# Optimization experiments

Hardware: AMD Instinct MI355X
Metric: run time of the kernel (lower is better)

## Reference

```python
import jax, jax.numpy as jnp
import numpy as np

B, N, D = 4, 4096, 256
H = 4
HD = D // H
FF = max(2 * D, 16)
EPS = 1e-5


def layer_norm(x, w, b):
    mu = jnp.mean(x, axis=-1, keepdims=True)
    var = jnp.mean(jnp.square(x - mu), axis=-1, keepdims=True)
    return (x - mu) * jax.lax.rsqrt(var + EPS) * w + b


def setup_inputs() -> dict:
    key = jax.random.key(0)
    ks = jax.random.split(key, 12)
    s = 1.0 / np.sqrt(D)
    sf = 1.0 / np.sqrt(FF)
    return {
        "tokens": jax.random.normal(ks[0], (B, N, D), jnp.float32),
        "importance": jax.random.normal(ks[1], (B, N), jnp.float32),
        "norm1_w": jnp.ones((D,), jnp.float32),
        "norm1_b": jnp.zeros((D,), jnp.float32),
        "Wq": jax.random.uniform(ks[2], (D, D), jnp.float32, -s, s),
        "bq": jnp.zeros((D,), jnp.float32),
        "Wk": jax.random.uniform(ks[3], (D, D), jnp.float32, -s, s),
        "bk": jnp.zeros((D,), jnp.float32),
        "Wv": jax.random.uniform(ks[4], (D, D), jnp.float32, -s, s),
        "bv": jnp.zeros((D,), jnp.float32),
        "Wo": jax.random.uniform(ks[5], (D, D), jnp.float32, -s, s),
        "bo": jnp.zeros((D,), jnp.float32),
        "norm2_w": jnp.ones((D,), jnp.float32),
        "norm2_b": jnp.zeros((D,), jnp.float32),
        "W1": jax.random.uniform(ks[6], (D, FF), jnp.float32, -s, s),
        "b1": jnp.zeros((FF,), jnp.float32),
        "W2": jax.random.uniform(ks[7], (FF, D), jnp.float32, -sf, sf),
        "b2": jnp.zeros((D,), jnp.float32),
    }


def reference(tokens, importance, norm1_w, norm1_b, Wq, bq, Wk, bk, Wv, bv,
              Wo, bo, norm2_w, norm2_b, W1, b1, W2, b2):
    # pre-norm MHA with additive importance bias
    x = layer_norm(tokens, norm1_w, norm1_b)
    q = (x @ Wq + bq).reshape(B, N, H, HD).transpose(0, 2, 1, 3)  # [B,H,N,HD]
    k = (x @ Wk + bk).reshape(B, N, H, HD).transpose(0, 2, 1, 3)
    v = (x @ Wv + bv).reshape(B, N, H, HD).transpose(0, 2, 1, 3)
    scores = jnp.einsum("bhnd,bhmd->bhnm", q, k) / np.sqrt(HD)
    scores = scores + importance[:, None, None, :]  # bias over key dim
    attn = jax.nn.softmax(scores, axis=-1)
    ctx = jnp.einsum("bhnm,bhmd->bhnd", attn, v)
    ctx = ctx.transpose(0, 2, 1, 3).reshape(B, N, D)
    x = tokens + (ctx @ Wo + bo)
    # GELU FFN (exact erf gelu, matching torch default)
    y = layer_norm(x, norm2_w, norm2_b)
    y = jax.nn.gelu(y @ W1 + b1, approximate=False) @ W2 + b2
    return x + y
```

## Files before the change

kernel.cpp:

```cpp
#include <hip/hip_runtime.h>

#define Bb 4
#define Nn 4096
#define Dd 256
#define Hh 4
#define HDd 64
#define FFf 512
#define MT 16384

typedef __attribute__((ext_vector_type(8))) short short8;
typedef __attribute__((ext_vector_type(4))) float f32x4;
typedef __attribute__((ext_vector_type(16))) float f32x16;
typedef unsigned short u16;
typedef unsigned int u32;
typedef __attribute__((ext_vector_type(4))) u32 u32x4;

typedef __attribute__((address_space(1))) const void glb_src;
typedef __attribute__((address_space(3))) void lds_dst;

__device__ __forceinline__ void gload_lds16(const void* g, void* l) {
    __builtin_amdgcn_global_load_lds((glb_src*)g, (lds_dst*)l, 16, 0, 0);
}

__device__ __forceinline__ u16 f2bf(float f) {
    union { float f; u32 i; } v; v.f = f;
    u32 r = v.i + 0x7FFFu + ((v.i >> 16) & 1u);
    return (u16)(r >> 16);
}

__device__ __forceinline__ short8 ld8(const u16* p) {
    return *(const short8*)p;
}

__device__ __forceinline__ void pl32swap(u32& a, u32& b) {
    asm("v_permlane32_swap_b32 %0, %1" : "+v"(a), "+v"(b));
}
__device__ __forceinline__ float xhalf_max(float x) {
    u32 a = __float_as_uint(x), b = a;
    pl32swap(a, b);
    return fmaxf(__uint_as_float(a), __uint_as_float(b));
}
__device__ __forceinline__ u32 cvtpk(float lo, float hi) {
    u32 r;
    asm("v_cvt_pk_bf16_f32 %0, %1, %2" : "=v"(r) : "v"(lo), "v"(hi));
    return r;
}
__device__ __forceinline__ float fexp2(float x) {
    float r;
    asm("v_exp_f32 %0, %1" : "=v"(r) : "v"(x));
    return r;
}
__device__ __forceinline__ float max3f(float a, float b, float c) {
    float r;
    asm("v_max3_f32 %0, %1, %2, %3" : "=v"(r) : "v"(a), "v"(b), "v"(c));
    return r;
}

#define QSCALE 0.18033610062f
#define LOG2E  1.44269504089f

__global__ __launch_bounds__(256) void prep_kernel(
        const float* __restrict__ Wq, const float* __restrict__ Wk,
        const float* __restrict__ Wv, const float* __restrict__ Wo,
        const float* __restrict__ W1, const float* __restrict__ W2,
        const float* __restrict__ imp,
        u16* __restrict__ WqkvT, u16* __restrict__ WoT,
        u16* __restrict__ W1T, u16* __restrict__ W2T,
        u32* __restrict__ impPk) {
    int e = blockIdx.x * 256 + threadIdx.x;
    if (e < 196608) {
        int c = e >> 8, k = e & 255;
        int mat = c >> 8;
        int cc = c & 255;
        const float* W = (mat == 0) ? Wq : ((mat == 1) ? Wk : Wv);
        WqkvT[(size_t)c * 256 + k] = f2bf(W[k * 256 + cc]);
    } else if (e < 262144) {
        int i = e - 196608; int n = i >> 8, k = i & 255;
        WoT[n * 256 + k] = f2bf(Wo[k * 256 + n]);
    } else if (e < 393216) {
        int i = e - 262144; int n = i >> 8, k = i & 255;
        W1T[n * 256 + k] = f2bf(W1[k * 512 + n]);
    } else if (e < 524288) {
        int i = e - 393216; int n = i >> 9, k = i & 511;
        W2T[n * 512 + k] = f2bf(W2[k * 256 + n]);
    } else {
        int i = e - 524288;
        float ivs = imp[i] * LOG2E;
        u16 ih = f2bf(ivs);
        float rem = ivs - __uint_as_float(((u32)ih) << 16);
        u16 il = f2bf(rem);
        impPk[i] = ((u32)il << 16) | ih;
    }
}

__global__ __launch_bounds__(256) void ln_kernel(const float* __restrict__ x,
        const float* __restrict__ w, const float* __restrict__ bia,
        u16* __restrict__ out) {
    int lane = threadIdx.x & 63;
    int row = blockIdx.x * 4 + (threadIdx.x >> 6);
    const float* xr = x + (size_t)row * Dd;
    float4 v = *(const float4*)(xr + lane * 4);
    float s = v.x + v.y + v.z + v.w;
    float s2 = v.x * v.x + v.y * v.y + v.z * v.z + v.w * v.w;
    #pragma unroll
    for (int off = 1; off < 64; off <<= 1) {
        s  += __shfl_xor(s, off);
        s2 += __shfl_xor(s2, off);
    }
    float mu = s * (1.0f / Dd);
    float var = s2 * (1.0f / Dd) - mu * mu;
    float rstd = rsqrtf(var + 1e-5f);
    float4 wv = *(const float4*)(w + lane * 4);
    float4 bv = *(const float4*)(bia + lane * 4);
    ushort4 ov;
    ov.x = f2bf((v.x - mu) * rstd * wv.x + bv.x);
    ov.y = f2bf((v.y - mu) * rstd * wv.y + bv.y);
    ov.z = f2bf((v.z - mu) * rstd * wv.z + bv.z);
    ov.w = f2bf((v.w - mu) * rstd * wv.w + bv.w);
    *(ushort4*)(out + (size_t)row * Dd + lane * 4) = ov;
}

template<int MODE, int KD>
__global__ __launch_bounds__(256) void gemm_bt(
        const u16* __restrict__ A, const u16* __restrict__ BT,
        const float* __restrict__ bias0, const float* __restrict__ bias1,
        const float* __restrict__ bias2,
        const float* __restrict__ resid, float* __restrict__ outf,
        u16* __restrict__ o0, u16* __restrict__ o1, u16* __restrict__ o2) {
    __shared__ u16 Asl[128 * 32];
    __shared__ u16 Bsl[128 * 32];
    int lane = threadIdx.x & 63;
    int wv = threadIdx.x >> 6;
    int wm = wv >> 1, wn = wv & 1;
    int m0 = blockIdx.y * 128, n0 = blockIdx.x * 128;
    f32x4 zz; zz[0] = 0.f; zz[1] = 0.f; zz[2] = 0.f; zz[3] = 0.f;
    f32x4 acc[4][4];
    #pragma unroll
    for (int i = 0; i < 4; ++i)
        #pragma unroll
        for (int j = 0; j < 4; ++j) acc[i][j] = zz;

    for (int kt = 0; kt < KD; kt += 32) {
        __syncthreads();
        #pragma unroll
        for (int i = 0; i < 2; ++i) {
            int chunk = threadIdx.x + i * 256;
            int row = chunk >> 2, c16 = chunk & 3;
            int lofs = row * 32 + ((c16 * 8) ^ ((row & 3) * 8));
            *(uint4*)(Asl + lofs) = *(const uint4*)(A + (size_t)(m0 + row) * KD + kt + c16 * 8);
            *(uint4*)(Bsl + lofs) = *(const uint4*)(BT + (size_t)(n0 + row) * KD + kt + c16 * 8);
        }
        __syncthreads();
        short8 af[4], bfr[4];
        #pragma unroll
        for (int t = 0; t < 4; ++t) {
            int arow = wm * 64 + t * 16 + (lane & 15);
            af[t]  = ld8(Asl + arow * 32 + (((lane >> 4) * 8) ^ ((arow & 3) * 8)));
            int brow = wn * 64 + t * 16 + (lane & 15);
            bfr[t] = ld8(Bsl + brow * 32 + (((lane >> 4) * 8) ^ ((brow & 3) * 8)));
        }
        #pragma unroll
        for (int mt = 0; mt < 4; ++mt)
            #pragma unroll
            for (int nt = 0; nt < 4; ++nt)
                acc[mt][nt] = __builtin_amdgcn_mfma_f32_16x16x32_bf16(af[mt], bfr[nt], acc[mt][nt], 0, 0, 0);
    }

    #pragma unroll
    for (int mt = 0; mt < 4; ++mt) {
        #pragma unroll
        for (int nt = 0; nt < 4; ++nt) {
            #pragma unroll
            for (int r = 0; r < 4; ++r) {
                int row = m0 + wm * 64 + mt * 16 + (lane >> 4) * 4 + r;
                int col = n0 + wn * 64 + nt * 16 + (lane & 15);
                float v = acc[mt][nt][r];
                if (MODE == 0) {
                    int mat = col >> 8;
                    int cc = col & 255;
                    int hh = cc >> 6, dd = cc & 63;
                    int bbi = row >> 12, nni = row & 4095;
                    int bh = bbi * Hh + hh;
                    if (mat == 0)      o0[((size_t)bh * Nn + nni) * HDd + dd] = f2bf((v + bias0[cc]) * QSCALE);
                    else if (mat == 1) o1[((size_t)bh * Nn + nni) * HDd + dd] = f2bf(v + bias1[cc]);
                    else               o2[((size_t)bh * HDd + dd) * Nn + nni] = f2bf(v + bias2[cc]);
                } else if (MODE == 1) {
                    outf[(size_t)row * Dd + col] = resid[(size_t)row * Dd + col] + v + bias0[col];
                } else if (MODE == 2) {
                    float xg = v + bias0[col];
                    float g = 0.5f * xg * (1.0f + erff(xg * 0.70710678118654752f));
                    o0[(size_t)row * FFf + col] = f2bf(g);
                } else {
                    outf[(size_t)row * Dd + col] = resid[(size_t)row * Dd + col] + v + bias0[col];
                }
            }
        }
    }
}

__global__ __launch_bounds__(256) void attn_kernel(
        const u16* __restrict__ Qb, const u16* __restrict__ Kb,
        const u16* __restrict__ VTb, const u32* __restrict__ impPk,
        u16* __restrict__ ctxOut) {
    __shared__ u16 Klds[2][64 * 64];
    __shared__ u16 Vlds[2][64 * 64];
    __shared__ float Clds[4][32 * 64];
    int lane = threadIdx.x & 63;
    int wv = threadIdx.x >> 6;
    int bh = blockIdx.x >> 5;
    int qt = blockIdx.x & 31;
    int bbi = bh >> 2, hh = bh & 3;
    int qrow0 = qt * 128 + wv * 32;
    int q = lane & 31;
    int hf = lane >> 5;

    short8 qf[4];
    #pragma unroll
    for (int ks = 0; ks < 4; ++ks)
        qf[ks] = ld8(Qb + ((size_t)bh * Nn + qrow0 + q) * HDd + ks * 16 + hf * 8);

    short8 onef = (short8)0;
    if (hf == 0) { onef[0] = (short)0x3F80; onef[1] = (short)0x3F80; }
    short8 aone;
    #pragma unroll
    for (int j = 0; j < 8; ++j) aone[j] = (short)0x3F80;

    int sr = lane >> 3;
    int sc = lane & 7;
    int swz = (sc ^ sr) * 8;
    const u16* kp = Kb + ((size_t)bh * Nn + wv * 16 + sr) * HDd + swz;
    const u16* vp = VTb + ((size_t)bh * HDd + wv * 16 + sr) * Nn + swz;
    size_t ib = (size_t)bbi * Nn;

    gload_lds16(kp,           (char*)Klds[0] + wv * 2048);
    gload_lds16(kp + 8 * HDd, (char*)Klds[0] + wv * 2048 + 1024);
    gload_lds16(vp,           (char*)Vlds[0] + wv * 2048);
    gload_lds16(vp + 8 * Nn,  (char*)Vlds[0] + wv * 2048 + 1024);
    kp += 64 * HDd; vp += 64;
    u32 npk0 = impPk[ib + q], npk1 = impPk[ib + 32 + q];

    f32x16 ctx[2], lacc;
    #pragma unroll
    for (int r = 0; r < 16; ++r) { ctx[0][r] = 0.f; ctx[1][r] = 0.f; lacc[r] = 0.f; }
    float m = -__builtin_inff();

    int cur = 0;
    for (int kt = 0; kt < Nn; kt += 64) {
        __syncthreads();
        u32 pk0 = npk0, pk1 = npk1;
        if (kt + 64 < Nn) {
            gload_lds16(kp,           (char*)Klds[cur ^ 1] + wv * 2048);
            gload_lds16(kp + 8 * HDd, (char*)Klds[cur ^ 1] + wv * 2048 + 1024);
            gload_lds16(vp,           (char*)Vlds[cur ^ 1] + wv * 2048);
            gload_lds16(vp + 8 * Nn,  (char*)Vlds[cur ^ 1] + wv * 2048 + 1024);
            kp += 64 * HDd; vp += 64;
            npk0 = impPk[ib + kt + 64 + q];
            npk1 = impPk[ib + kt + 96 + q];
        }
        const u16* Kc = Klds[cur];
        const u16* Vc = Vlds[cur];

        #pragma unroll
        for (int st = 0; st < 2; ++st) {
            int krow = st * 32 + q;
            f32x16 s;
            #pragma unroll
            for (int r = 0; r < 16; ++r) s[r] = 0.f;
            __builtin_amdgcn_s_setprio(1);
            #pragma unroll
            for (int ks = 0; ks < 4; ++ks) {
                short8 kf = ld8(Kc + krow * 64 + (((ks * 2 + hf) ^ (krow & 7)) * 8));
                s = __builtin_amdgcn_mfma_f32_32x32x16_bf16(kf, qf[ks], s, 0, 0, 0);
            }
            u32 pk = st ? pk1 : pk0;
            short8 af = (short8)0;
            if (hf == 0) { af[0] = (short)(pk & 0xFFFFu); af[1] = (short)(pk >> 16); }
            s = __builtin_amdgcn_mfma_f32_32x32x16_bf16(af, onef, s, 0, 0, 0);
            __builtin_amdgcn_s_setprio(0);

            float g0 = max3f(s[0], s[1], s[2]);
            float g1 = max3f(s[3], s[4], s[5]);
            float g2 = max3f(s[6], s[7], s[8]);
            float g3 = max3f(s[9], s[10], s[11]);
            float g4 = max3f(s[12], s[13], s[14]);
            float h0 = max3f(g0, g1, g2);
            float h1 = max3f(g3, g4, s[15]);
            float tm = xhalf_max(fmaxf(h0, h1));
            bool nore = __all(tm <= m + 8.0f);
            if (!nore) {
                float nm = fmaxf(m, tm);
                float al = fexp2(m - nm);
                lacc[0] *= al;
                #pragma unroll
                for (int r = 0; r < 16; ++r) { ctx[0][r] *= al; ctx[1][r] *= al; }
                m = nm;
            }
            #pragma unroll
            for (int r = 0; r < 16; ++r) s[r] = fexp2(s[r] - m);

            u32 w[8];
            #pragma unroll
            for (int j = 0; j < 8; ++j) w[j] = cvtpk(s[2 * j], s[2 * j + 1]);
            pl32swap(w[0], w[2]); pl32swap(w[1], w[3]);
            pl32swap(w[4], w[6]); pl32swap(w[5], w[7]);
            u32x4 t0; t0[0] = w[0]; t0[1] = w[1]; t0[2] = w[2]; t0[3] = w[3];
            u32x4 t1; t1[0] = w[4]; t1[1] = w[5]; t1[2] = w[6]; t1[3] = w[7];
            short8 pf0 = __builtin_bit_cast(short8, t0);
            short8 pf1 = __builtin_bit_cast(short8, t1);

            __builtin_amdgcn_s_setprio(1);
            lacc = __builtin_amdgcn_mfma_f32_32x32x16_bf16(aone, pf0, lacc, 0, 0, 0);
            lacc = __builtin_amdgcn_mfma_f32_32x32x16_bf16(aone, pf1, lacc, 0, 0, 0);
            #pragma unroll
            for (int dt = 0; dt < 2; ++dt) {
                int vrow = dt * 32 + q;
                short8 vf0 = ld8(Vc + vrow * 64 + (((st * 4 + hf) ^ (vrow & 7)) * 8));
                ctx[dt] = __builtin_amdgcn_mfma_f32_32x32x16_bf16(vf0, pf0, ctx[dt], 0, 0, 0);
                short8 vf1 = ld8(Vc + vrow * 64 + (((st * 4 + 2 + hf) ^ (vrow & 7)) * 8));
                ctx[dt] = __builtin_amdgcn_mfma_f32_32x32x16_bf16(vf1, pf1, ctx[dt], 0, 0, 0);
            }
            __builtin_amdgcn_s_setprio(0);
        }
        cur ^= 1;
    }

    float inv = 1.0f / lacc[0];
    #pragma unroll
    for (int dt = 0; dt < 2; ++dt) {
        #pragma unroll
        for (int r = 0; r < 16; ++r) {
            int d = dt * 32 + (r & 3) + 8 * (r >> 2) + 4 * hf;
            Clds[wv][q * 64 + (d ^ ((q & 7) << 2))] = ctx[dt][r] * inv;
        }
    }
    u16* op = ctxOut + ((size_t)bbi * Nn + qrow0 + q) * Dd + hh * HDd + hf * 32;
    #pragma unroll
    for (int gp = 0; gp < 4; ++gp) {
        int gi0 = hf * 8 + gp * 2, gi1 = gi0 + 1;
        int g0 = (gi0 & 8) | ((gi0 & 7) ^ (q & 7));
        int g1 = (gi1 & 8) | ((gi1 & 7) ^ (q & 7));
        float4 v0 = *(const float4*)(&Clds[wv][q * 64 + g0 * 4]);
        float4 v1 = *(const float4*)(&Clds[wv][q * 64 + g1 * 4]);
        uint4 pkv;
        pkv.x = cvtpk(v0.x, v0.y); pkv.y = cvtpk(v0.z, v0.w);
        pkv.z = cvtpk(v1.x, v1.y); pkv.w = cvtpk(v1.z, v1.w);
        *(uint4*)(op + gp * 8) = pkv;
    }
}

extern "C" void kernel_launch(void* const* d_in, const int* in_sizes, int n_in,
                              void* d_out, int out_size, void* d_ws, size_t ws_size,
                              hipStream_t stream) {
    (void)in_sizes; (void)n_in; (void)out_size; (void)ws_size;
    const float* tokens     = (const float*)d_in[0];
    const float* importance = (const float*)d_in[1];
    const float* n1w = (const float*)d_in[2];
    const float* n1b = (const float*)d_in[3];
    const float* Wq  = (const float*)d_in[4];
    const float* bq  = (const float*)d_in[5];
    const float* Wk  = (const float*)d_in[6];
    const float* bk  = (const float*)d_in[7];
    const float* Wv  = (const float*)d_in[8];
    const float* bv  = (const float*)d_in[9];
    const float* Wo  = (const float*)d_in[10];
    const float* bo  = (const float*)d_in[11];
    const float* n2w = (const float*)d_in[12];
    const float* n2b = (const float*)d_in[13];
    const float* W1  = (const float*)d_in[14];
    const float* b1  = (const float*)d_in[15];
    const float* W2  = (const float*)d_in[16];
    const float* b2  = (const float*)d_in[17];
    float* out = (float*)d_out;

    char* ws = (char*)d_ws;
    u16* xln   = (u16*)(ws);
    u16* qb    = (u16*)(ws + ((size_t)8 << 20));
    u16* kb    = (u16*)(ws + ((size_t)16 << 20));
    u16* vT    = (u16*)(ws + ((size_t)24 << 20));
    u16* ctx   = (u16*)(ws + ((size_t)32 << 20));
    float* x2  = (float*)(ws + ((size_t)40 << 20));
    u16* yln   = (u16*)(ws + ((size_t)56 << 20));
    u16* hbuf  = (u16*)(ws + ((size_t)64 << 20));
    u16* WqkvT = (u16*)(ws + ((size_t)80 << 20));
    u16* WoT   = (u16*)(ws + ((size_t)80 << 20) + 393216);
    u16* W1T   = (u16*)(ws + ((size_t)80 << 20) + 393216 + 131072);
    u16* W2T   = (u16*)(ws + ((size_t)80 << 20) + 393216 + 131072 + 262144);
    u32* impPk = (u32*)(ws + ((size_t)80 << 20) + 393216 + 131072 + 262144 + 262144);

    prep_kernel<<<2112, 256, 0, stream>>>(Wq, Wk, Wv, Wo, W1, W2, importance,
                                          WqkvT, WoT, W1T, W2T, impPk);
    ln_kernel<<<4096, 256, 0, stream>>>(tokens, n1w, n1b, xln);
    gemm_bt<0, 256><<<dim3(6, 128), 256, 0, stream>>>(xln, WqkvT, bq, bk, bv,
                                                      nullptr, nullptr, qb, kb, vT);
    attn_kernel<<<512, 256, 0, stream>>>(qb, kb, vT, impPk, ctx);
    gemm_bt<1, 256><<<dim3(2, 128), 256, 0, stream>>>(ctx, WoT, bo, nullptr, nullptr,
                                                      tokens, x2, nullptr, nullptr, nullptr);
    ln_kernel<<<4096, 256, 0, stream>>>(x2, n2w, n2b, yln);
    gemm_bt<2, 256><<<dim3(4, 128), 256, 0, stream>>>(yln, W1T, b1, nullptr, nullptr,
                                                      nullptr, nullptr, hbuf, nullptr, nullptr);
    gemm_bt<3, 512><<<dim3(2, 128), 256, 0, stream>>>(hbuf, W2T, b2, nullptr, nullptr,
                                                      x2, out, nullptr, nullptr, nullptr);
}
```

Before: 225.8 us.

## Split attention over two key halves with merge kernel; async LDS loads in GEMM

After: 202.2 us. 1.12x faster.

```diff
diff --git a/kernel.cpp b/kernel.cpp
--- a/kernel.cpp
+++ b/kernel.cpp
@@ -146,9 +146,11 @@
         for (int i = 0; i < 2; ++i) {
             int chunk = threadIdx.x + i * 256;
             int row = chunk >> 2, c16 = chunk & 3;
-            int lofs = row * 32 + ((c16 * 8) ^ ((row & 3) * 8));
-            *(uint4*)(Asl + lofs) = *(const uint4*)(A + (size_t)(m0 + row) * KD + kt + c16 * 8);
-            *(uint4*)(Bsl + lofs) = *(const uint4*)(BT + (size_t)(n0 + row) * KD + kt + c16 * 8);
+            int srcc = (c16 ^ (row & 3)) * 8;
+            char* adst = (char*)Asl + wv * 1024 + i * 4096;
+            char* bdst = (char*)Bsl + wv * 1024 + i * 4096;
+            gload_lds16(A  + (size_t)(m0 + row) * KD + kt + srcc, adst);
+            gload_lds16(BT + (size_t)(n0 + row) * KD + kt + srcc, bdst);
         }
         __syncthreads();
         short8 af[4], bfr[4];
@@ -198,21 +200,22 @@
     }
 }
 
-__global__ __launch_bounds__(256) void attn_kernel(
+__global__ __launch_bounds__(256, 4) void attn_kernel(
         const u16* __restrict__ Qb, const u16* __restrict__ Kb,
         const u16* __restrict__ VTb, const u32* __restrict__ impPk,
-        u16* __restrict__ ctxOut) {
+        u16* __restrict__ pc, float* __restrict__ pm, float* __restrict__ pl) {
     __shared__ u16 Klds[2][64 * 64];
     __shared__ u16 Vlds[2][64 * 64];
-    __shared__ float Clds[4][32 * 64];
     int lane = threadIdx.x & 63;
     int wv = threadIdx.x >> 6;
-    int bh = blockIdx.x >> 5;
+    int kvh = blockIdx.x >> 9;
+    int bh = (blockIdx.x >> 5) & 15;
     int qt = blockIdx.x & 31;
-    int bbi = bh >> 2, hh = bh & 3;
+    int bbi = bh >> 2;
     int qrow0 = qt * 128 + wv * 32;
     int q = lane & 31;
     int hf = lane >> 5;
+    int key0 = kvh * 2048;
 
     short8 qf[4];
     #pragma unroll
@@ -228,8 +231,8 @@
     int sr = lane >> 3;
     int sc = lane & 7;
     int swz = (sc ^ sr) * 8;
-    const u16* kp = Kb + ((size_t)bh * Nn + wv * 16 + sr) * HDd + swz;
-    const u16* vp = VTb + ((size_t)bh * HDd + wv * 16 + sr) * Nn + swz;
+    const u16* kp = Kb + ((size_t)bh * Nn + key0 + wv * 16 + sr) * HDd + swz;
+    const u16* vp = VTb + ((size_t)bh * HDd + wv * 16 + sr) * Nn + key0 + swz;
     size_t ib = (size_t)bbi * Nn;
 
     gload_lds16(kp,           (char*)Klds[0] + wv * 2048);
@@ -237,7 +240,7 @@
     gload_lds16(vp,           (char*)Vlds[0] + wv * 2048);
     gload_lds16(vp + 8 * Nn,  (char*)Vlds[0] + wv * 2048 + 1024);
     kp += 64 * HDd; vp += 64;
-    u32 npk0 = impPk[ib + q], npk1 = impPk[ib + 32 + q];
+    u32 npk0 = impPk[ib + key0 + q], npk1 = impPk[ib + key0 + 32 + q];
 
     f32x16 ctx[2], lacc;
     #pragma unroll
@@ -245,107 +248,167 @@
     float m = -__builtin_inff();
 
     int cur = 0;
-    for (int kt = 0; kt < Nn; kt += 64) {
+    for (int t = 0; t < 32; ++t) {
         __syncthreads();
         u32 pk0 = npk0, pk1 = npk1;
-        if (kt + 64 < Nn) {
+        if (t < 31) {
             gload_lds16(kp,           (char*)Klds[cur ^ 1] + wv * 2048);
             gload_lds16(kp + 8 * HDd, (char*)Klds[cur ^ 1] + wv * 2048 + 1024);
             gload_lds16(vp,           (char*)Vlds[cur ^ 1] + wv * 2048);
             gload_lds16(vp + 8 * Nn,  (char*)Vlds[cur ^ 1] + wv * 2048 + 1024);
             kp += 64 * HDd; vp += 64;
-            npk0 = impPk[ib + kt + 64 + q];
-            npk1 = impPk[ib + kt + 96 + q];
+            npk0 = impPk[ib + key0 + t * 64 + 64 + q];
+            npk1 = impPk[ib + key0 + t * 64 + 96 + q];
         }
         const u16* Kc = Klds[cur];
         const u16* Vc = Vlds[cur];
 
-        #pragma unroll
-        for (int st = 0; st < 2; ++st) {
-            int krow = st * 32 + q;
-            f32x16 s;
+        f32x16 s0, s1;
+        #pragma unroll
+        for (int r = 0; r < 16; ++r) { s0[r] = 0.f; s1[r] = 0.f; }
+        __builtin_amdgcn_s_setprio(1);
+        #pragma unroll
+        for (int ks = 0; ks < 4; ++ks) {
+            short8 kf0 = ld8(Kc + q * 64 + (((ks * 2 + hf) ^ (q & 7)) * 8));
+            short8 kf1 = ld8(Kc + (32 + q) * 64 + (((ks * 2 + hf) ^ (q & 7)) * 8));
+            s0 = __builtin_amdgcn_mfma_f32_32x32x16_bf16(kf0, qf[ks], s0, 0, 0, 0);
+            s1 = __builtin_amdgcn_mfma_f32_32x32x16_bf16(kf1, qf[ks], s1, 0, 0, 0);
+        }
+        short8 af0 = (short8)0, af1 = (short8)0;
+        if (hf == 0) {
+            af0[0] = (short)(pk0 & 0xFFFFu); af0[1] = (short)(pk0 >> 16);
+            af1[0] = (short)(pk1 & 0xFFFFu); af1[1] = (short)(pk1 >> 16);
+        }
+        s0 = __builtin_amdgcn_mfma_f32_32x32x16_bf16(af0, onef, s0, 0, 0, 0);
+        s1 = __builtin_amdgcn_mfma_f32_32x32x16_bf16(af1, onef, s1, 0, 0, 0);
+        __builtin_amdgcn_s_setprio(0);
+
+        float a0 = max3f(s0[0], s0[1], s0[2]);
+        float a1 = max3f(s0[3], s0[4], s0[5]);
+        float a2 = max3f(s0[6], s0[7], s0[8]);
+        float a3 = max3f(s0[9], s0[10], s0[11]);
+        float a4 = max3f(s0[12], s0[13], s0[14]);
+        float b0 = max3f(s1[0], s1[1], s1[2]);
+        float b1 = max3f(s1[3], s1[4], s1[5]);
+        float b2 = max3f(s1[6], s1[7], s1[8]);
+        float b3 = max3f(s1[9], s1[10], s1[11]);
+        float b4 = max3f(s1[12], s1[13], s1[14]);
+        float c0 = max3f(a0, a1, a2);
+        float c1 = max3f(a3, a4, s0[15]);
+        float c2 = max3f(b0, b1, b2);
+        float c3 = max3f(b3, b4, s1[15]);
+        float tm = fmaxf(max3f(c0, c1, c2), c3);
+        tm = xhalf_max(tm);
+        bool nore = __all(tm <= m + 8.0f);
+        if (!nore) {
+            float nm = fmaxf(m, tm);
+            float al = fexp2(m - nm);
+            lacc[0] *= al;
             #pragma unroll
-            for (int r = 0; r < 16; ++r) s[r] = 0.f;
-            __builtin_amdgcn_s_setprio(1);
-            #pragma unroll
-            for (int ks = 0; ks < 4; ++ks) {
-                short8 kf = ld8(Kc + krow * 64 + (((ks * 2 + hf) ^ (krow & 7)) * 8));
-                s = __builtin_amdgcn_mfma_f32_32x32x16_bf16(kf, qf[ks], s, 0, 0, 0);
-            }
-            u32 pk = st ? pk1 : pk0;
-            short8 af = (short8)0;
-            if (hf == 0) { af[0] = (short)(pk & 0xFFFFu); af[1] = (short)(pk >> 16); }
-            s = __builtin_amdgcn_mfma_f32_32x32x16_bf16(af, onef, s, 0, 0, 0);
-            __builtin_amdgcn_s_setprio(0);
-
-            float g0 = max3f(s[0], s[1], s[2]);
-            float g1 = max3f(s[3], s[4], s[5]);
-            float g2 = max3f(s[6], s[7], s[8]);
-            float g3 = max3f(s[9], s[10], s[11]);
-            float g4 = max3f(s[12], s[13], s[14]);
-            float h0 = max3f(g0, g1, g2);
-            float h1 = max3f(g3, g4, s[15]);
-            float tm = xhalf_max(fmaxf(h0, h1));
-            bool nore = __all(tm <= m + 8.0f);
-            if (!nore) {
-                float nm = fmaxf(m, tm);
-                float al = fexp2(m - nm);
-                lacc[0] *= al;
-                #pragma unroll
-                for (int r = 0; r < 16; ++r) { ctx[0][r] *= al; ctx[1][r] *= al; }
-                m = nm;
-            }
-            #pragma unroll
-            for (int r = 0; r < 16; ++r) s[r] = fexp2(s[r] - m);
-
-            u32 w[8];
-            #pragma unroll
-            for (int j = 0; j < 8; ++j) w[j] = cvtpk(s[2 * j], s[2 * j + 1]);
-            pl32swap(w[0], w[2]); pl32swap(w[1], w[3]);
-            pl32swap(w[4], w[6]); pl32swap(w[5], w[7]);
-            u32x4 t0; t0[0] = w[0]; t0[1] = w[1]; t0[2] = w[2]; t0[3] = w[3];
-            u32x4 t1; t1[0] = w[4]; t1[1] = w[5]; t1[2] = w[6]; t1[3] = w[7];
-            short8 pf0 = __builtin_bit_cast(short8, t0);
-            short8 pf1 = __builtin_bit_cast(short8, t1);
-
-            __builtin_amdgcn_s_setprio(1);
-            lacc = __builtin_amdgcn_mfma_f32_32x32x16_bf16(aone, pf0, lacc, 0, 0, 0);
-            lacc = __builtin_amdgcn_mfma_f32_32x32x16_bf16(aone, pf1, lacc, 0, 0, 0);
-            #pragma unroll
-            for (int dt = 0; dt < 2; ++dt) {
-                int vrow = dt * 32 + q;
-                short8 vf0 = ld8(Vc + vrow * 64 + (((st * 4 + hf) ^ (vrow & 7)) * 8));
-                ctx[dt] = __builtin_amdgcn_mfma_f32_32x32x16_bf16(vf0, pf0, ctx[dt], 0, 0, 0);
-                short8 vf1 = ld8(Vc + vrow * 64 + (((st * 4 + 2 + hf) ^ (vrow & 7)) * 8));
-                ctx[dt] = __builtin_amdgcn_mfma_f32_32x32x16_bf16(vf1, pf1, ctx[dt], 0, 0, 0);
-            }
-            __builtin_amdgcn_s_setprio(0);
-        }
+            for (int r = 0; r < 16; ++r) { ctx[0][r] *= al; ctx[1][r] *= al; }
+            m = nm;
+        }
+        #pragma unroll
+        for (int r = 0; r < 16; ++r) { s0[r] = fexp2(s0[r] - m); s1[r] = fexp2(s1[r] - m); }
+
+        u32 w0[8], w1[8];
+        #pragma unroll
+        for (int j = 0; j < 8; ++j) {
+            w0[j] = cvtpk(s0[2 * j], s0[2 * j + 1]);
+            w1[j] = cvtpk(s1[2 * j], s1[2 * j + 1]);
+        }
+        pl32swap(w0[0], w0[2]); pl32swap(w0[1], w0[3]);
+        pl32swap(w0[4], w0[6]); pl32swap(w0[5], w0[7]);
+        pl32swap(w1[0], w1[2]); pl32swap(w1[1], w1[3]);
+        pl32swap(w1[4], w1[6]); pl32swap(w1[5], w1[7]);
+        u32x4 t00; t00[0] = w0[0]; t00[1] = w0[1]; t00[2] = w0[2]; t00[3] = w0[3];
+        u32x4 t01; t01[0] = w0[4]; t01[1] = w0[5]; t01[2] = w0[6]; t01[3] = w0[7];
+        u32x4 t10; t10[0] = w1[0]; t10[1] = w1[1]; t10[2] = w1[2]; t10[3] = w1[3];
+        u32x4 t11; t11[0] = w1[4]; t11[1] = w1[5]; t11[2] = w1[6]; t11[3] = w1[7];
+        short8 pf00 = __builtin_bit_cast(short8, t00);
+        short8 pf01 = __builtin_bit_cast(short8, t01);
+        short8 pf10 = __builtin_bit_cast(short8, t10);
+        short8 pf11 = __builtin_bit_cast(short8, t11);
+
+        __builtin_amdgcn_s_setprio(1);
+        lacc = __builtin_amdgcn_mfma_f32_32x32x16_bf16(aone, pf00, lacc, 0, 0, 0);
+        lacc = __builtin_amdgcn_mfma_f32_32x32x16_bf16(aone, pf01, lacc, 0, 0, 0);
+        lacc = __builtin_amdgcn_mfma_f32_32x32x16_bf16(aone, pf10, lacc, 0, 0, 0);
+        lacc = __builtin_amdgcn_mfma_f32_32x32x16_bf16(aone, pf11, lacc, 0, 0, 0);
+        #pragma unroll
+        for (int dt = 0; dt < 2; ++dt) {
+            int vrow = dt * 32 + q;
+            const u16* vb = Vc + vrow * 64;
+            int sw = vrow & 7;
+            short8 vf;
+            vf = ld8(vb + (((0 + hf) ^ sw) * 8));
+            ctx[dt] = __builtin_amdgcn_mfma_f32_32x32x16_bf16(vf, pf00, ctx[dt], 0, 0, 0);
+            vf = ld8(vb + (((2 + hf) ^ sw) * 8));
+            ctx[dt] = __builtin_amdgcn_mfma_f32_32x32x16_bf16(vf, pf01, ctx[dt], 0, 0, 0);
+            vf = ld8(vb + (((4 + hf) ^ sw) * 8));
+            ctx[dt] = __builtin_amdgcn_mfma_f32_32x32x16_bf16(vf, pf10, ctx[dt], 0, 0, 0);
+            vf = ld8(vb + (((6 + hf) ^ sw) * 8));
+            ctx[dt] = __builtin_amdgcn_mfma_f32_32x32x16_bf16(vf, pf11, ctx[dt], 0, 0, 0);
+        }
+        __builtin_amdgcn_s_setprio(0);
         cur ^= 1;
     }
 
-    float inv = 1.0f / lacc[0];
+    int qg = qrow0 + q;
+    if (hf == 0) {
+        pm[(size_t)(kvh * 16 + bh) * Nn + qg] = m;
+        pl[(size_t)(kvh * 16 + bh) * Nn + qg] = lacc[0];
+    }
     #pragma unroll
     for (int dt = 0; dt < 2; ++dt) {
         #pragma unroll
         for (int r = 0; r < 16; ++r) {
             int d = dt * 32 + (r & 3) + 8 * (r >> 2) + 4 * hf;
-            Clds[wv][q * 64 + (d ^ ((q & 7) << 2))] = ctx[dt][r] * inv;
-        }
-    }
-    u16* op = ctxOut + ((size_t)bbi * Nn + qrow0 + q) * Dd + hh * HDd + hf * 32;
-    #pragma unroll
-    for (int gp = 0; gp < 4; ++gp) {
-        int gi0 = hf * 8 + gp * 2, gi1 = gi0 + 1;
-        int g0 = (gi0 & 8) | ((gi0 & 7) ^ (q & 7));
-        int g1 = (gi1 & 8) | ((gi1 & 7) ^ (q & 7));
-        float4 v0 = *(const float4*)(&Clds[wv][q * 64 + g0 * 4]);
-        float4 v1 = *(const float4*)(&Clds[wv][q * 64 + g1 * 4]);
-        uint4 pkv;
-        pkv.x = cvtpk(v0.x, v0.y); pkv.y = cvtpk(v0.z, v0.w);
-        pkv.z = cvtpk(v1.x, v1.y); pkv.w = cvtpk(v1.z, v1.w);
-        *(uint4*)(op + gp * 8) = pkv;
-    }
+            pc[((size_t)(kvh * 16 + bh) * 64 + d) * Nn + qg] = f2bf(ctx[dt][r]);
+        }
+    }
+}
+
+__global__ __launch_bounds__(256) void merge_kernel(
+        const u16* __restrict__ pc, const float* __restrict__ pm,
+        const float* __restrict__ pl, u16* __restrict__ ctxOut) {
+    __shared__ float trans[64][65];
+    __shared__ float f0a[64], f1a[64];
+    int bh = blockIdx.x >> 6;
+    int q0 = (blockIdx.x & 63) * 64;
+    int t = threadIdx.x;
+    if (t < 64) {
+        int qg = q0 + t;
+        float m0 = pm[(size_t)bh * Nn + qg];
+        float m1 = pm[(size_t)(16 + bh) * Nn + qg];
+        float l0 = pl[(size_t)bh * Nn + qg];
+        float l1 = pl[(size_t)(16 + bh) * Nn + qg];
+        float M = fmaxf(m0, m1);
+        float w0 = fexp2(m0 - M), w1 = fexp2(m1 - M);
+        float inv = 1.0f / (l0 * w0 + l1 * w1);
+        f0a[t] = w0 * inv; f1a[t] = w1 * inv;
+    }
+    __syncthreads();
+    int wv = t >> 6, lane = t & 63;
+    #pragma unroll
+    for (int i = 0; i < 16; ++i) {
+        int d = wv * 16 + i;
+        float c0 = __uint_as_float((u32)pc[((size_t)bh * 64 + d) * Nn + q0 + lane] << 16);
+        float c1 = __uint_as_float((u32)pc[((size_t)(16 + bh) * 64 + d) * Nn + q0 + lane] << 16);
+        trans[lane][d] = c0 * f0a[lane] + c1 * f1a[lane];
+    }
+    __syncthreads();
+    int q = t >> 2, dg = t & 3;
+    int b = bh >> 2, h = bh & 3;
+    const float* tr = &trans[q][dg * 16];
+    uint4 pa, pb;
+    pa.x = cvtpk(tr[0], tr[1]);  pa.y = cvtpk(tr[2], tr[3]);
+    pa.z = cvtpk(tr[4], tr[5]);  pa.w = cvtpk(tr[6], tr[7]);
+    pb.x = cvtpk(tr[8], tr[9]);  pb.y = cvtpk(tr[10], tr[11]);
+    pb.z = cvtpk(tr[12], tr[13]); pb.w = cvtpk(tr[14], tr[15]);
+    u16* op = ctxOut + ((size_t)b * Nn + q0 + q) * Dd + h * 64 + dg * 16;
+    *(uint4*)op = pa;
+    *(uint4*)(op + 8) = pb;
 }
 
 extern "C" void kernel_launch(void* const* d_in, const int* in_sizes, int n_in,
@@ -373,26 +436,31 @@
     float* out = (float*)d_out;
 
     char* ws = (char*)d_ws;
+    const size_t MB = (size_t)1 << 20;
     u16* xln   = (u16*)(ws);
-    u16* qb    = (u16*)(ws + ((size_t)8 << 20));
-    u16* kb    = (u16*)(ws + ((size_t)16 << 20));
-    u16* vT    = (u16*)(ws + ((size_t)24 << 20));
-    u16* ctx   = (u16*)(ws + ((size_t)32 << 20));
-    float* x2  = (float*)(ws + ((size_t)40 << 20));
-    u16* yln   = (u16*)(ws + ((size_t)56 << 20));
-    u16* hbuf  = (u16*)(ws + ((size_t)64 << 20));
-    u16* WqkvT = (u16*)(ws + ((size_t)80 << 20));
-    u16* WoT   = (u16*)(ws + ((size_t)80 << 20) + 393216);
-    u16* W1T   = (u16*)(ws + ((size_t)80 << 20) + 393216 + 131072);
-    u16* W2T   = (u16*)(ws + ((size_t)80 << 20) + 393216 + 131072 + 262144);
-    u32* impPk = (u32*)(ws + ((size_t)80 << 20) + 393216 + 131072 + 262144 + 262144);
+    u16* qb    = (u16*)(ws + 8 * MB);
+    u16* kb    = (u16*)(ws + 16 * MB);
+    u16* vT    = (u16*)(ws + 24 * MB);
+    u16* ctx   = (u16*)(ws + 32 * MB);
+    u16* pc    = (u16*)(ws + 40 * MB);
+    float* pm  = (float*)(ws + 56 * MB);
+    float* pl  = (float*)(ws + 56 * MB + 524288);
+    u16* WqkvT = (u16*)(ws + 57 * MB);
+    u16* WoT   = (u16*)(ws + 57 * MB + 393216);
+    u16* W1T   = (u16*)(ws + 57 * MB + 393216 + 131072);
+    u16* W2T   = (u16*)(ws + 57 * MB + 393216 + 131072 + 262144);
+    u32* impPk = (u32*)(ws + 57 * MB + 393216 + 131072 + 262144 + 262144);
+    u16* yln   = xln;
+    u16* hbuf  = qb;
+    float* x2  = out;
 
     prep_kernel<<<2112, 256, 0, stream>>>(Wq, Wk, Wv, Wo, W1, W2, importance,
                                           WqkvT, WoT, W1T, W2T, impPk);
     ln_kernel<<<4096, 256, 0, stream>>>(tokens, n1w, n1b, xln);
     gemm_bt<0, 256><<<dim3(6, 128), 256, 0, stream>>>(xln, WqkvT, bq, bk, bv,
                                                       nullptr, nullptr, qb, kb, vT);
-    attn_kernel<<<512, 256, 0, stream>>>(qb, kb, vT, impPk, ctx);
+    attn_kernel<<<1024, 256, 0, stream>>>(qb, kb, vT, impPk, pc, pm, pl);
+    merge_kernel<<<1024, 256, 0, stream>>>(pc, pm, pl, ctx);
     gemm_bt<1, 256><<<dim3(2, 128), 256, 0, stream>>>(ctx, WoT, bo, nullptr, nullptr,
                                                       tokens, x2, nullptr, nullptr, nullptr);
     ln_kernel<<<4096, 256, 0, stream>>>(x2, n2w, n2b, yln);
```
